# Kernel optimization log

Hardware: AMD Instinct MI355X
Metric: run time of the kernel (lower is better)

Reference implementation:

```python
import jax, jax.numpy as jnp
import numpy as np

ORIENTATIONS = 8
CELL = 16          # pixels_per_cell = (16, 16)
EPS = 1e-5         # skimage L2-Hys eps


def _hog_features(x):
    """x: [B, H, W, C] float image. Faithful to skimage.feature.hog with
    orientations=8, pixels_per_cell=(16,16), cells_per_block=(1,1),
    block_norm='L2-Hys', multichannel gradient selection."""
    B, H, W, C = x.shape
    # per-channel central-difference gradients, zero at borders (skimage _hog_channel_gradient)
    g_row = jnp.zeros_like(x).at[:, 1:-1, :, :].set(x[:, 2:, :, :] - x[:, :-2, :, :])
    g_col = jnp.zeros_like(x).at[:, :, 1:-1, :].set(x[:, :, 2:, :] - x[:, :, :-2, :])
    magn_ch = jnp.hypot(g_row, g_col)                      # [B,H,W,C]
    # pick channel with max gradient magnitude per pixel
    idx = jnp.argmax(magn_ch, axis=-1, keepdims=True)      # [B,H,W,1]
    gr = jnp.take_along_axis(g_row, idx, axis=-1)[..., 0]  # [B,H,W]
    gc = jnp.take_along_axis(g_col, idx, axis=-1)[..., 0]
    magn = jnp.take_along_axis(magn_ch, idx, axis=-1)[..., 0]
    # orientation in degrees, mod 180 (unsigned gradients)
    ori = jnp.degrees(jnp.arctan2(gr, gc)) % 180.0
    bin_width = 180.0 / ORIENTATIONS
    bin_idx = jnp.clip(jnp.floor(ori / bin_width).astype(jnp.int32), 0, ORIENTATIONS - 1)
    ncr, ncc = H // CELL, W // CELL
    # per-cell mean magnitude for each orientation bin
    hists = []
    for o in range(ORIENTATIONS):
        m = jnp.where(bin_idx == o, magn, 0.0)             # [B,H,W]
        m = m.reshape(B, ncr, CELL, ncc, CELL).mean(axis=(2, 4))  # [B,ncr,ncc]
        hists.append(m)
    hist = jnp.stack(hists, axis=-1)                       # [B,ncr,ncc,O]
    # block normalization: 1x1 cells per block, 'L2-Hys'
    n = hist / jnp.sqrt(jnp.sum(hist * hist, axis=-1, keepdims=True) + EPS ** 2)
    n = jnp.minimum(n, 0.2)
    n = n / jnp.sqrt(jnp.sum(n * n, axis=-1, keepdims=True) + EPS ** 2)
    return n.reshape(B, -1)                                # [B, ncr*ncc*O]


def setup_inputs() -> dict:
    key = jax.random.key(0)
    fake = jax.random.uniform(key, (64, 3, 512, 512), dtype=jnp.float32)
    return {"fake": fake}


def reference(fake) -> jnp.ndarray:
    x = jnp.transpose(fake, (0, 2, 3, 1))  # NCHW -> NHWC (module's permute)
    return _hog_features(x)
```

## Files before the change

kernel.cpp:

```cpp
#include <hip/hip_runtime.h>
#include <math.h>


namespace {

constexpr int Hh = 512;
constexpr int Ww = 512;
constexpr int CHN = 3;
constexpr int HW = Hh * Ww;
constexpr float TAN22 = 0.41421356237309503f;

__global__ __launch_bounds__(256, 4) void hog_kernel(const float* __restrict__ x,
                                                     float* __restrict__ out) {
    const int b       = blockIdx.x >> 6;
    const int cellrow = (blockIdx.x >> 1) & 31;
    const int colhalf = blockIdx.x & 1;
    const int tx      = threadIdx.x;
    const int lane    = tx & 63;
    const int wid     = tx >> 6;
    const int r0      = cellrow * 16 + wid * 4;
    const int c0      = colhalf << 8;

    const float* xb = x + (size_t)b * (CHN * HW);

    float4 R[6][CHN];
#pragma unroll
    for (int r = 0; r < 6; ++r) {
        int h = r0 - 1 + r;
        h = h < 0 ? 0 : (h > Hh - 1 ? Hh - 1 : h);
#pragma unroll
        for (int ch = 0; ch < CHN; ++ch)
            R[r][ch] = *(const float4*)(xb + (size_t)ch * HW +
                                        (size_t)h * Ww + c0 + (lane << 2));
    }

    float halov = 0.f;
    if (lane < 24) {
        const int ch = lane >> 3, r = (lane >> 1) & 3, side = lane & 1;
        int wcol = side ? c0 + 256 : c0 - 1;
        wcol = wcol < 0 ? 0 : (wcol > Ww - 1 ? Ww - 1 : wcol);
        halov = xb[(size_t)ch * HW + (size_t)(r0 + r) * Ww + wcol];
    }

    const bool bL = (colhalf == 0) & (lane == 0);
    const bool bR = (colhalf == 1) & (lane == 63);

    float c[8];
#pragma unroll
    for (int o = 0; o < 8; ++o) c[o] = 0.f;

#pragma unroll
    for (int hh = 0; hh < 4; ++hh) {
        const int h = r0 + hh;
        const bool rowEdge = (h == 0) | (h == Hh - 1);

        float gL[CHN], gR[CHN];
#pragma unroll
        for (int ch = 0; ch < CHN; ++ch) {
            const float su = __shfl_up(R[hh + 1][ch].w, 1, 64);
            const float sd = __shfl_down(R[hh + 1][ch].x, 1, 64);
            const float hl = __shfl(halov, (ch << 3) | (hh << 1), 64);
            const float hr = __shfl(halov, (ch << 3) | (hh << 1) | 1, 64);
            gL[ch] = (lane == 0)  ? hl : su;
            gR[ch] = (lane == 63) ? hr : sd;
        }

#pragma unroll
        for (int i = 0; i < 4; ++i) {
            float bm2 = -1.f, bgr = 0.f, bgc = 0.f;
#pragma unroll
            for (int ch = 0; ch < CHN; ++ch) {
                const float4 pv = R[hh][ch];
                const float4 cv = R[hh + 1][ch];
                const float4 nv = R[hh + 2][ch];
                const float pr_[4] = {pv.x, pv.y, pv.z, pv.w};
                const float cu_[4] = {cv.x, cv.y, cv.z, cv.w};
                const float nx_[4] = {nv.x, nv.y, nv.z, nv.w};
                const float gl  = (i == 0) ? gL[ch] : cu_[i - 1];
                const float gr_ = (i == 3) ? gR[ch] : cu_[i + 1];
                float gcol = gr_ - gl;
                if (i == 0) gcol = bL ? 0.f : gcol;
                if (i == 3) gcol = bR ? 0.f : gcol;
                float gv = nx_[i] - pr_[i];
                gv = rowEdge ? 0.f : gv;
                const float m2 = fmaf(gv, gv, gcol * gcol);
                if (m2 > bm2) { bm2 = m2; bgr = gv; bgc = gcol; }
            }
            const float m = sqrtf(bm2);

            const bool flip = (bgr < 0.f) | ((bgr == 0.f) & (bgc < 0.f));
            const float bb = flip ? -bgr : bgr;
            const float A  = flip ? -bgc : bgc;
            const float Aa = fabsf(A);
            const float p1 = Aa * TAN22;
            const float p2 = bb * TAN22;
            const bool q2  = (A <= 0.f);
            const bool ge1 = (bb >= p1), ge2 = (bb >= Aa), ge3 = (p2 >= Aa);
            const bool gt1 = (bb > p1),  gt2 = (bb > Aa),  gt3 = (p2 > Aa);
            c[0] += m;
            c[1] += (q2 | ge1) ? m : 0.f;
            c[2] += (q2 | ge2) ? m : 0.f;
            c[3] += (q2 | ge3) ? m : 0.f;
            c[4] += q2 ? m : 0.f;
            c[5] += (q2 & !gt3) ? m : 0.f;
            c[6] += (q2 & !gt2) ? m : 0.f;
            c[7] += (q2 & !gt1) ? m : 0.f;
        }
    }

#pragma unroll
    for (int o = 0; o < 8; ++o) {
        c[o] += __shfl_xor(c[o], 1, 64);
        c[o] += __shfl_xor(c[o], 2, 64);
    }

    __shared__ float lh[4][16][9];
    if (tx < 64) lh[tx >> 4][tx & 15][8] = 0.f;
    if ((lane & 3) == 0) {
        const int cell = lane >> 2;
#pragma unroll
        for (int o = 0; o < 8; ++o) lh[wid][cell][o] = c[o];
    }
    __syncthreads();

    if (tx < 128) {
        const int cell = tx >> 3;
        const int o    = tx & 7;
        const float c_o  = lh[0][cell][o]     + lh[1][cell][o] +
                           lh[2][cell][o]     + lh[3][cell][o];
        const float c_o1 = lh[0][cell][o + 1] + lh[1][cell][o + 1] +
                           lh[2][cell][o + 1] + lh[3][cell][o + 1];
        const float hv = (c_o - c_o1) * (1.0f / 256.0f);

        float ss = hv * hv;
        ss += __shfl_xor(ss, 1, 64);
        ss += __shfl_xor(ss, 2, 64);
        ss += __shfl_xor(ss, 4, 64);
        float n1 = hv / sqrtf(ss + 1e-10f);
        n1 = fminf(n1, 0.2f);
        float s2 = n1 * n1;
        s2 += __shfl_xor(s2, 1, 64);
        s2 += __shfl_xor(s2, 2, 64);
        s2 += __shfl_xor(s2, 4, 64);
        const float nv = n1 / sqrtf(s2 + 1e-10f);

        out[(((size_t)b * 32 + cellrow) * 32 + (colhalf * 16 + cell)) * 8 + o] = nv;
    }
}

}

extern "C" void kernel_launch(void* const* d_in, const int* in_sizes, int n_in,
                              void* d_out, int out_size, void* d_ws, size_t ws_size,
                              hipStream_t stream) {
    (void)n_in; (void)out_size; (void)d_ws; (void)ws_size;
    const float* x = (const float*)d_in[0];
    float* out = (float*)d_out;
    const int B = in_sizes[0] / (CHN * HW);
    const int grid = B * 32 * 2;
    hog_kernel<<<grid, 256, 0, stream>>>(x, out);
}
```

Baseline: 269.1 us.

## Remap HOG kernel to one pixel column per thread with 4x more blocks

```diff
diff --git a/kernel.cpp b/kernel.cpp
--- a/kernel.cpp
+++ b/kernel.cpp
@@ -10,40 +10,40 @@
 constexpr int HW = Hh * Ww;
 constexpr float TAN22 = 0.41421356237309503f;
 
-__global__ __launch_bounds__(256, 4) void hog_kernel(const float* __restrict__ x,
+__global__ __launch_bounds__(256, 6) void hog_kernel(const float* __restrict__ x,
                                                      float* __restrict__ out) {
-    const int b       = blockIdx.x >> 6;
-    const int cellrow = (blockIdx.x >> 1) & 31;
-    const int colhalf = blockIdx.x & 1;
-    const int tx      = threadIdx.x;
-    const int lane    = tx & 63;
-    const int wid     = tx >> 6;
-    const int r0      = cellrow * 16 + wid * 4;
-    const int c0      = colhalf << 8;
+    const int b    = blockIdx.x >> 8;
+    const int cr   = (blockIdx.x >> 3) & 31;
+    const int cg   = blockIdx.x & 7;
+    const int tx   = threadIdx.x;
+    const int lane = tx & 63;
+    const int wid  = tx >> 6;
+    const int r0   = cr * 16 + wid * 4;
+    const int w    = cg * 64 + lane;
 
     const float* xb = x + (size_t)b * (CHN * HW);
 
-    float4 R[6][CHN];
+    const int wl = (w == 0) ? 0 : w - 1;
+    const int wr = (w == Ww - 1) ? Ww - 1 : w + 1;
+    const bool colEdge = (w == 0) | (w == Ww - 1);
+
+    float V[CHN][6];
+    float Lv[CHN][4], Rv[CHN][4];
 #pragma unroll
-    for (int r = 0; r < 6; ++r) {
-        int h = r0 - 1 + r;
-        h = h < 0 ? 0 : (h > Hh - 1 ? Hh - 1 : h);
+    for (int ch = 0; ch < CHN; ++ch) {
 #pragma unroll
-        for (int ch = 0; ch < CHN; ++ch)
-            R[r][ch] = *(const float4*)(xb + (size_t)ch * HW +
-                                        (size_t)h * Ww + c0 + (lane << 2));
+        for (int r = 0; r < 6; ++r) {
+            int h = r0 - 1 + r;
+            h = h < 0 ? 0 : (h > Hh - 1 ? Hh - 1 : h);
+            V[ch][r] = xb[(size_t)ch * HW + (size_t)h * Ww + w];
+        }
+#pragma unroll
+        for (int r = 0; r < 4; ++r) {
+            const float* rowp = xb + (size_t)ch * HW + (size_t)(r0 + r) * Ww;
+            Lv[ch][r] = rowp[wl];
+            Rv[ch][r] = rowp[wr];
+        }
     }
-
-    float halov = 0.f;
-    if (lane < 24) {
-        const int ch = lane >> 3, r = (lane >> 1) & 3, side = lane & 1;
-        int wcol = side ? c0 + 256 : c0 - 1;
-        wcol = wcol < 0 ? 0 : (wcol > Ww - 1 ? Ww - 1 : wcol);
-        halov = xb[(size_t)ch * HW + (size_t)(r0 + r) * Ww + wcol];
-    }
-
-    const bool bL = (colhalf == 0) & (lane == 0);
-    const bool bR = (colhalf == 1) & (lane == 63);
 
     float c[8];
 #pragma unroll
@@ -54,76 +54,55 @@
         const int h = r0 + hh;
         const bool rowEdge = (h == 0) | (h == Hh - 1);
 
-        float gL[CHN], gR[CHN];
+        float bm2 = -1.f, bgr = 0.f, bgc = 0.f;
 #pragma unroll
         for (int ch = 0; ch < CHN; ++ch) {
-            const float su = __shfl_up(R[hh + 1][ch].w, 1, 64);
-            const float sd = __shfl_down(R[hh + 1][ch].x, 1, 64);
-            const float hl = __shfl(halov, (ch << 3) | (hh << 1), 64);
-            const float hr = __shfl(halov, (ch << 3) | (hh << 1) | 1, 64);
-            gL[ch] = (lane == 0)  ? hl : su;
-            gR[ch] = (lane == 63) ? hr : sd;
+            float gv = V[ch][hh + 2] - V[ch][hh];
+            gv = rowEdge ? 0.f : gv;
+            float gc_ = Rv[ch][hh] - Lv[ch][hh];
+            gc_ = colEdge ? 0.f : gc_;
+            const float m2 = fmaf(gv, gv, gc_ * gc_);
+            if (m2 > bm2) { bm2 = m2; bgr = gv; bgc = gc_; }
         }
+        const float m = sqrtf(bm2);
 
-#pragma unroll
-        for (int i = 0; i < 4; ++i) {
-            float bm2 = -1.f, bgr = 0.f, bgc = 0.f;
-#pragma unroll
-            for (int ch = 0; ch < CHN; ++ch) {
-                const float4 pv = R[hh][ch];
-                const float4 cv = R[hh + 1][ch];
-                const float4 nv = R[hh + 2][ch];
-                const float pr_[4] = {pv.x, pv.y, pv.z, pv.w};
-                const float cu_[4] = {cv.x, cv.y, cv.z, cv.w};
-                const float nx_[4] = {nv.x, nv.y, nv.z, nv.w};
-                const float gl  = (i == 0) ? gL[ch] : cu_[i - 1];
-                const float gr_ = (i == 3) ? gR[ch] : cu_[i + 1];
-                float gcol = gr_ - gl;
-                if (i == 0) gcol = bL ? 0.f : gcol;
-                if (i == 3) gcol = bR ? 0.f : gcol;
-                float gv = nx_[i] - pr_[i];
-                gv = rowEdge ? 0.f : gv;
-                const float m2 = fmaf(gv, gv, gcol * gcol);
-                if (m2 > bm2) { bm2 = m2; bgr = gv; bgc = gcol; }
-            }
-            const float m = sqrtf(bm2);
-
-            const bool flip = (bgr < 0.f) | ((bgr == 0.f) & (bgc < 0.f));
-            const float bb = flip ? -bgr : bgr;
-            const float A  = flip ? -bgc : bgc;
-            const float Aa = fabsf(A);
-            const float p1 = Aa * TAN22;
-            const float p2 = bb * TAN22;
-            const bool q2  = (A <= 0.f);
-            const bool ge1 = (bb >= p1), ge2 = (bb >= Aa), ge3 = (p2 >= Aa);
-            const bool gt1 = (bb > p1),  gt2 = (bb > Aa),  gt3 = (p2 > Aa);
-            c[0] += m;
-            c[1] += (q2 | ge1) ? m : 0.f;
-            c[2] += (q2 | ge2) ? m : 0.f;
-            c[3] += (q2 | ge3) ? m : 0.f;
-            c[4] += q2 ? m : 0.f;
-            c[5] += (q2 & !gt3) ? m : 0.f;
-            c[6] += (q2 & !gt2) ? m : 0.f;
-            c[7] += (q2 & !gt1) ? m : 0.f;
-        }
+        const bool flip = (bgr < 0.f) | ((bgr == 0.f) & (bgc < 0.f));
+        const float bb = flip ? -bgr : bgr;
+        const float A  = flip ? -bgc : bgc;
+        const float Aa = fabsf(A);
+        const float p1 = Aa * TAN22;
+        const float p2 = bb * TAN22;
+        const bool q2  = (A <= 0.f);
+        const bool ge1 = (bb >= p1), ge2 = (bb >= Aa), ge3 = (p2 >= Aa);
+        const bool gt1 = (bb > p1),  gt2 = (bb > Aa),  gt3 = (p2 > Aa);
+        c[0] += m;
+        c[1] += (q2 | ge1) ? m : 0.f;
+        c[2] += (q2 | ge2) ? m : 0.f;
+        c[3] += (q2 | ge3) ? m : 0.f;
+        c[4] += q2 ? m : 0.f;
+        c[5] += (q2 & !gt3) ? m : 0.f;
+        c[6] += (q2 & !gt2) ? m : 0.f;
+        c[7] += (q2 & !gt1) ? m : 0.f;
     }
 
 #pragma unroll
     for (int o = 0; o < 8; ++o) {
         c[o] += __shfl_xor(c[o], 1, 64);
         c[o] += __shfl_xor(c[o], 2, 64);
+        c[o] += __shfl_xor(c[o], 4, 64);
+        c[o] += __shfl_xor(c[o], 8, 64);
     }
 
-    __shared__ float lh[4][16][9];
-    if (tx < 64) lh[tx >> 4][tx & 15][8] = 0.f;
-    if ((lane & 3) == 0) {
-        const int cell = lane >> 2;
+    __shared__ float lh[4][4][9];
+    if (tx < 16) lh[tx >> 2][tx & 3][8] = 0.f;
+    if ((lane & 15) == 0) {
+        const int cell = lane >> 4;
 #pragma unroll
         for (int o = 0; o < 8; ++o) lh[wid][cell][o] = c[o];
     }
     __syncthreads();
 
-    if (tx < 128) {
+    if (tx < 32) {
         const int cell = tx >> 3;
         const int o    = tx & 7;
         const float c_o  = lh[0][cell][o]     + lh[1][cell][o] +
@@ -144,7 +123,7 @@
         s2 += __shfl_xor(s2, 4, 64);
         const float nv = n1 / sqrtf(s2 + 1e-10f);
 
-        out[(((size_t)b * 32 + cellrow) * 32 + (colhalf * 16 + cell)) * 8 + o] = nv;
+        out[(((size_t)b * 32 + cr) * 32 + (cg * 4 + cell)) * 8 + o] = nv;
     }
 }
 
@@ -157,6 +136,6 @@
     const float* x = (const float*)d_in[0];
     float* out = (float*)d_out;
     const int B = in_sizes[0] / (CHN * HW);
-    const int grid = B * 32 * 2;
+    const int grid = B * 32 * 8;
     hog_kernel<<<grid, 256, 0, stream>>>(x, out);
 }
```

Result: slower. 275.1 us (+2.2%).
